# Optimization experiments

Hardware: AMD Instinct MI355X
Metric: run time of the kernel (lower is better)

Reference implementation:

```python
import jax, jax.numpy as jnp
import numpy as np
from jax import lax

BLOCK = 64      # block_size
OVERLAP = 16
NITER = 64      # Niter init kwarg; loop runs min(1000, Niter)
L = 0.24        # diffusion step size
K = 0.03        # exp(logk), logk = log(0.03)
DEPS = 0.1
FFT_STEPS = 10
THRESH = 0.1    # uniform-region variance threshold


def _g(x):
    # g(x) = 1 / (1 + |x^2| / K^2)
    return 1.0 / (1.0 + jnp.abs(x * x) / (K * K))


def _avgpool3(x):
    # F.avg_pool2d(x, 3, stride=1, padding=1) with count_include_pad=True (divide by 9)
    s = lax.reduce_window(x, 0.0, lax.add, (1, 1, 3, 3), (1, 1, 1, 1),
                          [(0, 0), (0, 0), (1, 1), (1, 1)])
    return s / 9.0


def _fft_diffuse_block(block, bcv, bch):
    cv_mean = bcv.mean()
    ch_mean = bch.mean()
    h, w = block.shape[2], block.shape[3]
    ky = jnp.arange(h, dtype=block.dtype)[:, None] * (2.0 * np.pi / h)      # [h,1]
    kx = jnp.arange(w // 2 + 1, dtype=block.dtype)[None, :] * (2.0 * np.pi / w)  # [1,w//2+1]
    op = (1.0 - 2.0 * L * (cv_mean * (1.0 - jnp.cos(ky)) + ch_mean * (1.0 - jnp.cos(kx)))) ** FFT_STEPS
    return jnp.fft.irfft2(jnp.fft.rfft2(block) * op, s=(h, w))


def _forward(guide, initial):
    # depth shift for stability (torch code branches on initial.min() <= deps)
    shift = jnp.where(initial.min() <= DEPS, DEPS, 0.0).astype(initial.dtype)
    depth = initial + shift

    # diffusion coefficients from guide: cv [B,1,H-1,W], ch [B,1,H,W-1]
    cv = _g(jnp.mean(jnp.abs(guide[:, :, 1:, :] - guide[:, :, :-1, :]), axis=1, keepdims=True))
    ch = _g(jnp.mean(jnp.abs(guide[:, :, :, 1:] - guide[:, :, :, :-1]), axis=1, keepdims=True))

    # identify_uniform_regions (local variance via avg pools); original torch code
    # broadcasts shapes (H-1,W) & (H,W-1) which errors -- we crop to common (H-1,W-1)
    cv_var = _avgpool3(cv ** 2) - _avgpool3(cv) ** 2
    ch_var = _avgpool3(ch ** 2) - _avgpool3(ch) ** 2
    uniform = ((cv_var[:, :, :, :-1] < THRESH) & (ch_var[:, :, :-1, :] < THRESH)).astype(depth.dtype)

    B, C, H, W = depth.shape
    step = BLOCK - OVERLAP
    # sequential per-block FFT diffusion with overlap blending (blocks read
    # depth updated by previous blocks, so order matters)
    for b in range(B):
        for y in range(0, H, step):
            for x in range(0, W, step):
                y_end = min(y + BLOCK, H)
                x_end = min(x + BLOCK, W)
                bh, bw = y_end - y, x_end - x
                block = depth[b:b + 1, :, y:y_end, x:x_end]
                bcv = cv[b:b + 1, :, y:y_end - 1, x:x_end]
                bch = ch[b:b + 1, :, y:y_end, x:x_end - 1]
                bun = uniform[b:b + 1, :, y:y_end, x:x_end]  # clips at edges (H-1,W-1)
                cond = bun.mean() > 0.7
                newb = _fft_diffuse_block(block, bcv, bch)
                if y > 0 or x > 0:
                    blend_y = jnp.ones((bh,), depth.dtype)
                    if y > 0:
                        r = jnp.arange(bh)
                        blend_y = jnp.where(r < min(OVERLAP, bh), r.astype(depth.dtype) / OVERLAP, blend_y)
                    blend_x = jnp.ones((bw,), depth.dtype)
                    if x > 0:
                        r = jnp.arange(bw)
                        blend_x = jnp.where(r < min(OVERLAP, bw), r.astype(depth.dtype) / OVERLAP, blend_x)
                    blend = (blend_y[:, None] * blend_x[None, :])[None, None]
                    cand = block * (1.0 - blend) + newb * blend
                else:
                    cand = newb
                region = jnp.where(cond, cand, block)
                depth = depth.at[b:b + 1, :, y:y_end, x:x_end].set(region)

    # explicit anisotropic diffusion stencil, serial data dependence -> lax.scan
    def diffuse_step(I, _):
        dv = I[:, :, 1:, :] - I[:, :, :-1, :]
        dh = I[:, :, :, 1:] - I[:, :, :, :-1]  # computed before vertical update (as in torch)
        tv = L * cv * dv
        I = I.at[:, :, 1:, :].add(-tv).at[:, :, :-1, :].add(tv)
        th = L * ch * dh
        I = I.at[:, :, :, 1:].add(-th).at[:, :, :, :-1].add(th)
        return I, None

    depth, _ = lax.scan(diffuse_step, depth, None, length=min(1000, NITER))
    y_pred = depth - shift
    return y_pred, cv, ch


def setup_inputs() -> dict:
    key = jax.random.key(0)
    k1, k2 = jax.random.split(key)
    guide = jax.random.uniform(k1, (2, 3, 512, 512), dtype=jnp.float32)
    initial = jax.random.uniform(k2, (2, 1, 512, 512), dtype=jnp.float32)
    return {"guide": guide, "initial": initial}


def reference(guide, initial):
    # returns (y_pred, cv, ch) matching {'y_pred':..., 'cv':..., 'ch':...}
    return _forward(guide, initial)
```

## Files before the change

### kernel.cpp

```cpp
#include <hip/hip_runtime.h>
#include <stdint.h>

#define LDIFF 0.24f

constexpr int H = 512, W = 512, NB = 2;
constexpr int HW = H * W;
constexpr int N_D = NB * HW;
constexpr int CVH = 511, CVW = 512;
constexpr int CHH = 512, CHW = 511;
constexpr int N_CV = NB * CVH * CVW;
constexpr int NBLKS = 11;
constexpr int NBT = NB * 121;

__device__ inline float ldc(const float* p) {
    return __hip_atomic_load(p, __ATOMIC_RELAXED, __HIP_MEMORY_SCOPE_AGENT);
}
__device__ inline void stc(float* p, float v) {
    __hip_atomic_store(p, v, __ATOMIC_RELAXED, __HIP_MEMORY_SCOPE_AGENT);
}
__device__ inline void poll_ge(const int* p, int v) {
    while (__hip_atomic_load(p, __ATOMIC_RELAXED, __HIP_MEMORY_SCOPE_AGENT) < v)
        __builtin_amdgcn_s_sleep(2);
}

__device__ inline float rot_a(float x) {
    return __int_as_float(__builtin_amdgcn_update_dpp(0, __float_as_int(x), 0x134, 0xf, 0xf, false));
}
__device__ inline float rot_b(float x) {
    return __int_as_float(__builtin_amdgcn_update_dpp(0, __float_as_int(x), 0x13c, 0xf, 0xf, false));
}
__device__ inline float sh_a(float x) {
    return __int_as_float(__builtin_amdgcn_update_dpp(0, __float_as_int(x), 0x130, 0xf, 0xf, true));
}
__device__ inline float sh_b(float x) {
    return __int_as_float(__builtin_amdgcn_update_dpp(0, __float_as_int(x), 0x138, 0xf, 0xf, true));
}

__global__ __launch_bounds__(256) void kall(
    const float* __restrict__ guide, const float* __restrict__ initial,
    float* __restrict__ cv, float* __restrict__ ch,
    float* __restrict__ D, float* __restrict__ T0, float* __restrict__ T1,
    float* __restrict__ ypred, int* __restrict__ sync_)
{
    __shared__ float pool[8712];
    __shared__ float sm[256];
    __shared__ float prmS[3];
    __shared__ float xT[4][64];
    __shared__ float xB[4][64];
    __shared__ float cvB[4][64];
    float* cvT = pool;
    float* chT = pool + 4356;

    int* wflag = sync_;
    int* dflag = sync_ + 4096;
    int* bar   = sync_ + 8192;

    const int blk = blockIdx.x;
    const int i = blk / NBLKS, j = blk % NBLKS;
    const int b = blockIdx.y;
    const int tid = threadIdx.x;
    const int lane = tid & 63, wv = tid >> 6;
    const int r0 = wv * 16;
    const int me = b * 121 + blk;

    const float kinv = 1.0f / (0.03f * 0.03f);
    for (int idx = me * 256 + tid; idx < N_D; idx += NBT * 256) {
        int bb = idx >> 18;
        int yx = idx & (HW - 1);
        int y = yx >> 9, x = yx & 511;
        const float* g = guide + (size_t)bb * 3 * HW + yx;
        float g0 = g[0], g1 = g[HW], g2 = g[2 * HW];
        stc(&D[idx], initial[idx]);
        if (y < 511) {
            float d = (fabsf(g[512] - g0) + fabsf(g[HW + 512] - g1) + fabsf(g[2 * HW + 512] - g2)) * (1.0f / 3.0f);
            cv[bb * CVH * CVW + y * CVW + x] = 1.0f / (1.0f + d * d * kinv);
        }
        if (x < 511) {
            float d = (fabsf(g[1] - g0) + fabsf(g[HW + 1] - g1) + fabsf(g[2 * HW + 1] - g2)) * (1.0f / 3.0f);
            ch[bb * CHH * CHW + y * CHW + x] = 1.0f / (1.0f + d * d * kinv);
        }
    }

    __syncthreads();
    if (tid == 0) {
        __hip_atomic_fetch_add(bar, 1, __ATOMIC_ACQ_REL, __HIP_MEMORY_SCOPE_AGENT);
        while (__hip_atomic_load(bar, __ATOMIC_RELAXED, __HIP_MEMORY_SCOPE_AGENT) < NBT)
            __builtin_amdgcn_s_sleep(8);
    }
    __syncthreads();
    __builtin_amdgcn_fence(__ATOMIC_ACQUIRE, "agent");

    const int y0 = i * 48, x0 = j * 48;
    const int y1 = min(y0 + 64, 512), x1 = min(x0 + 64, 512);
    const int bh = y1 - y0, bw = x1 - x0;
    const float* cvb = cv + b * CVH * CVW;
    const float* chb = ch + b * CHH * CHW;

    for (int p = tid; p < 66 * 66; p += 256) {
        int rr = p / 66, c2 = p - rr * 66;
        int y = y0 - 1 + rr, x = x0 - 1 + c2;
        cvT[p] = (y >= 0 && y < 511 && x >= 0 && x < 512) ? cvb[y * CVW + x] : 0.0f;
        chT[p] = (y >= 0 && y < 512 && x >= 0 && x < 511) ? chb[y * CHW + x] : 0.0f;
    }
    __syncthreads();

    float scv = 0.f, sch = 0.f, sun = 0.f;
    {
        int n = (bh - 1) * bw;
        for (int p = tid; p < n; p += 256) { int r = p / bw, c = p - r * bw; scv += cvT[(r + 1) * 66 + c + 1]; }
    }
    {
        int cols = bw - 1, n = bh * cols;
        for (int p = tid; p < n; p += 256) { int r = p / cols, c = p - r * cols; sch += chT[(r + 1) * 66 + c + 1]; }
    }
    const int ur = min(y1, 511) - y0, uc = min(x1, 511) - x0;
    {
        int n = ur * uc;
        for (int p = tid; p < n; p += 256) {
            int r = p / uc, c = p - r * uc;
            float s1 = 0.f, s2 = 0.f, t1 = 0.f, t2 = 0.f;
            #pragma unroll
            for (int dy = 0; dy < 3; dy++)
                #pragma unroll
                for (int dx = 0; dx < 3; dx++) {
                    float v = cvT[(r + dy) * 66 + c + dx]; s1 += v; s2 += v * v;
                    float w2 = chT[(r + dy) * 66 + c + dx]; t1 += w2; t2 += w2 * w2;
                }
            float m = s1 * (1.0f / 9.0f);
            float vcv = s2 * (1.0f / 9.0f) - m * m;
            m = t1 * (1.0f / 9.0f);
            float vch = t2 * (1.0f / 9.0f) - m * m;
            if (vcv < 0.1f && vch < 0.1f) sun += 1.f;
        }
    }
    sm[tid] = scv; __syncthreads();
    for (int s = 128; s; s >>= 1) { if (tid < s) sm[tid] += sm[tid + s]; __syncthreads(); }
    if (tid == 0) prmS[0] = sm[0] / (float)((bh - 1) * bw);
    __syncthreads();
    sm[tid] = sch; __syncthreads();
    for (int s = 128; s; s >>= 1) { if (tid < s) sm[tid] += sm[tid + s]; __syncthreads(); }
    if (tid == 0) prmS[1] = sm[0] / (float)(bh * (bw - 1));
    __syncthreads();
    sm[tid] = sun; __syncthreads();
    for (int s = 128; s; s >>= 1) { if (tid < s) sm[tid] += sm[tid + s]; __syncthreads(); }
    if (tid == 0) prmS[2] = (sm[0] / (float)(ur * uc) > 0.7f) ? 1.0f : 0.0f;
    __syncthreads();

    const bool docond = prmS[2] > 0.5f;
    if (tid == 0 && !docond)
        __hip_atomic_store(&wflag[me * 16], 1, __ATOMIC_RELAXED, __HIP_MEMORY_SCOPE_AGENT);

    int pr = __builtin_amdgcn_update_dpp(0, lane, 0x134, 0xf, 0xf, false);
    const bool dirL = (pr == ((lane + 63) & 63));

    float* Db = D + b * HW;
    const float* ini = initial + b * HW;

    if (docond) {
        const float a = LDIFF * prmS[0], bc = LDIFF * prmS[1];
        const int mh = bh - 1, mw = bw - 1;
        const int cc = lane & mw;
        float u[16], orig[16];
        int addr[16]; bool fD[16];
        #pragma unroll
        for (int k = 0; k < 16; k++) {
            int rr = (r0 + k) & mh;
            addr[k] = (y0 + rr) * W + x0 + cc;
            fD[k] = (i > 0 && rr < 16) || (j > 0 && cc < 16);
            if (!fD[k]) orig[k] = ini[addr[k]];
        }
        if (tid < 4) {
            int di = (tid == 0) ? i : i - 1;
            int dj = (tid == 0) ? j - 1 : j - 2 + tid;
            if (di >= 0 && dj >= 0 && dj < NBLKS)
                poll_ge(&wflag[(b * 121 + di * NBLKS + dj) * 16], 1);
        }
        __syncthreads();
        #pragma unroll
        for (int k = 0; k < 16; k++) if (fD[k]) orig[k] = ldc(&Db[addr[k]]);
        #pragma unroll
        for (int k = 0; k < 16; k++) u[k] = orig[k];

        for (int it = 0; it < 10; it++) {
            xT[wv][lane] = u[0];
            xB[wv][lane] = u[15];
            __syncthreads();
            float ub = xB[(wv + 3) & 3][lane];
            float ut = xT[(wv + 1) & 3][lane];
            float nu[16];
            #pragma unroll
            for (int k = 0; k < 16; k++) {
                float up = (k == 0) ? ub : u[k - 1];
                float dn = (k == 15) ? ut : u[k + 1];
                float hsum = rot_a(u[k]) + rot_b(u[k]);
                nu[k] = u[k] + a * (up + dn - 2.0f * u[k]) + bc * (hsum - 2.0f * u[k]);
            }
            #pragma unroll
            for (int k = 0; k < 16; k++) u[k] = nu[k];
            __syncthreads();
        }

        if (lane < bw) {
            float bxw = (x0 > 0 && lane < 16) ? (float)lane * (1.0f / 16.0f) : 1.0f;
            #pragma unroll
            for (int k = 0; k < 16; k++) {
                int r = r0 + k;
                if (r < bh) {
                    float byw = (y0 > 0 && r < 16) ? (float)r * (1.0f / 16.0f) : 1.0f;
                    float wgt = byw * bxw;
                    stc(&Db[(y0 + r) * W + x0 + lane], orig[k] * (1.0f - wgt) + u[k] * wgt);
                }
            }
        }
        asm volatile("s_waitcnt vmcnt(0)" ::: "memory");
        __syncthreads();
        if (tid == 0)
            __hip_atomic_store(&wflag[me * 16], 1, __ATOMIC_RELAXED, __HIP_MEMORY_SCOPE_AGENT);
    }

    const int gy0 = y0 - 8, gx0 = x0 - 8;
    const int cx = gx0 + lane;
    const int gxc = min(max(cx, 0), 511);
    const bool xv = (cx >= 0 && cx < 512);
    float cvr[16], chr[16], chl[16];
    int gyA[16];
    #pragma unroll
    for (int k = 0; k < 16; k++) {
        int cy = gy0 + r0 + k;
        gyA[k] = min(max(cy, 0), 511);
        cvr[k] = (cy >= 0 && cy < 511 && xv) ? cvb[cy * CVW + cx] : 0.0f;
        chr[k] = (cy >= 0 && cy < 512 && xv && cx < 511) ? chb[cy * CHW + cx] : 0.0f;
        chl[k] = dirL ? sh_a(chr[k]) : sh_b(chr[k]);
    }
    cvB[wv][lane] = cvr[15];
    __syncthreads();
    const float cvm1 = (wv == 0) ? 0.0f : cvB[wv - 1][lane];

    float* Tb0 = T0 + b * HW;
    float* Tb1 = T1 + b * HW;
    float* ypb = ypred + b * HW;
    const bool cok = (lane >= 8 && lane < 56 && gx0 + lane < 512);

    for (int t = 1; t <= 8; t++) {
        if (tid < 9) {
            int di = tid / 3 - 1, dj = tid % 3 - 1;
            if (di != 0 || dj != 0) {
                int ni = i + di, nj = j + dj;
                if (ni >= 0 && ni < NBLKS && nj >= 0 && nj < NBLKS) {
                    int nb = (b * 121 + ni * NBLKS + nj) * 16;
                    if (t == 1) poll_ge(&wflag[nb], 1);
                    else        poll_ge(&dflag[nb], t - 1);
                }
            }
        }
        __syncthreads();
        const float* src = (t == 1) ? Db : (((t - 1) & 1) ? Tb1 : Tb0);
        float u[16];
        #pragma unroll
        for (int k = 0; k < 16; k++) u[k] = ldc(&src[gyA[k] * W + gxc]);

        for (int it = 0; it < 8; it++) {
            xT[wv][lane] = u[0];
            xB[wv][lane] = u[15];
            __syncthreads();
            float ub = (wv > 0) ? xB[wv - 1][lane] : u[0];
            float ut = (wv < 3) ? xT[wv + 1][lane] : u[15];
            float V[16];
            #pragma unroll
            for (int k = 0; k < 16; k++) {
                float up = (k == 0) ? ub : u[k - 1];
                float dn = (k == 15) ? ut : u[k + 1];
                float cup = (k == 0) ? cvm1 : cvr[k - 1];
                V[k] = u[k] + LDIFF * cvr[k] * (dn - u[k]) - LDIFF * cup * (u[k] - up);
            }
            #pragma unroll
            for (int k = 0; k < 16; k++) {
                float rA = rot_a(V[k]);
                float rB = rot_b(V[k]);
                float lf = dirL ? rA : rB;
                float rt = dirL ? rB : rA;
                u[k] = V[k] + LDIFF * chr[k] * (rt - V[k]) - LDIFF * chl[k] * (V[k] - lf);
            }
            __syncthreads();
        }

        if (t < 8) {
            float* dst = (t & 1) ? Tb1 : Tb0;
            if (cok) {
                #pragma unroll
                for (int k = 0; k < 16; k++) {
                    int r = r0 + k;
                    if (r >= 8 && r < 56) {
                        int y = gy0 + r;
                        if (y < 512) stc(&dst[y * W + gx0 + lane], u[k]);
                    }
                }
            }
            asm volatile("s_waitcnt vmcnt(0)" ::: "memory");
            __syncthreads();
            if (tid == 0)
                __hip_atomic_store(&dflag[me * 16], t, __ATOMIC_RELAXED, __HIP_MEMORY_SCOPE_AGENT);
        } else {
            if (cok) {
                #pragma unroll
                for (int k = 0; k < 16; k++) {
                    int r = r0 + k;
                    if (r >= 8 && r < 56) {
                        int y = gy0 + r;
                        if (y < 512) ypb[y * W + gx0 + lane] = u[k];
                    }
                }
            }
        }
    }
}

extern "C" void kernel_launch(void* const* d_in, const int* in_sizes, int n_in,
                              void* d_out, int out_size, void* d_ws, size_t ws_size,
                              hipStream_t stream) {
    const float* guide   = (const float*)d_in[0];
    const float* initial = (const float*)d_in[1];
    float* y_pred = (float*)d_out;
    float* cv = y_pred + N_D;
    float* ch = cv + N_CV;

    uint8_t* w = (uint8_t*)d_ws;
    int* sync_ = (int*)w;
    float* D  = (float*)(w + 36864);
    float* T0 = (float*)(w + 36864 + (size_t)N_D * 4);
    float* T1 = (float*)(w + 36864 + (size_t)2 * N_D * 4);

    hipMemsetAsync(sync_, 0, 36864, stream);
    kall<<<dim3(121, NB), 256, 0, stream>>>(guide, initial, cv, ch, D, T0, T1, y_pred, sync_);
}
```

Measured before the change: 351.3 us.

## Serialize block-row FFT phase in one workgroup per row with LDS strip handoff

The sequential per-block smoothing phase is reassigned so that the first workgroup of each block row processes all 11 blocks of that row in order. Other workgroups publish their block statistics through a global parameter queue, and the row worker passes the 16-column overlap strip to the next block through shared memory. Per-block flags are replaced by per-row progress counters, which removes cross-workgroup flag round trips and repeated global reloads of the overlap region. In exchange, most workgroups sit idle while the row workers run serially, and the stencil phase now waits on row progress instead of neighbouring block flags.

Result: slower. 449.1 us (+27.8%).

```diff
diff --git a/kernel.cpp b/kernel.cpp
--- a/kernel.cpp
+++ b/kernel.cpp
@@ -18,9 +18,15 @@
 __device__ inline void stc(float* p, float v) {
     __hip_atomic_store(p, v, __ATOMIC_RELAXED, __HIP_MEMORY_SCOPE_AGENT);
 }
+__device__ inline int ldci(const int* p) {
+    return __hip_atomic_load(p, __ATOMIC_RELAXED, __HIP_MEMORY_SCOPE_AGENT);
+}
+__device__ inline void stci(int* p, int v) {
+    __hip_atomic_store(p, v, __ATOMIC_RELAXED, __HIP_MEMORY_SCOPE_AGENT);
+}
+template <int SLP>
 __device__ inline void poll_ge(const int* p, int v) {
-    while (__hip_atomic_load(p, __ATOMIC_RELAXED, __HIP_MEMORY_SCOPE_AGENT) < v)
-        __builtin_amdgcn_s_sleep(2);
+    while (ldci(p) < v) __builtin_amdgcn_s_sleep(SLP);
 }
 
 __device__ inline float rot_a(float x) {
@@ -44,16 +50,18 @@
 {
     __shared__ float pool[8712];
     __shared__ float sm[256];
-    __shared__ float prmS[3];
+    __shared__ float prmS[4];
     __shared__ float xT[4][64];
     __shared__ float xB[4][64];
     __shared__ float cvB[4][64];
+    __shared__ float stripS[64][16];
     float* cvT = pool;
     float* chT = pool + 4356;
 
-    int* wflag = sync_;
-    int* dflag = sync_ + 4096;
-    int* bar   = sync_ + 8192;
+    int* bar     = sync_;
+    int* rowflag = sync_ + 16;
+    int* dflag   = sync_ + 512;
+    int* prmq    = sync_ + 4608;
 
     const int blk = blockIdx.x;
     const int i = blk / NBLKS, j = blk % NBLKS;
@@ -84,8 +92,7 @@
     __syncthreads();
     if (tid == 0) {
         __hip_atomic_fetch_add(bar, 1, __ATOMIC_ACQ_REL, __HIP_MEMORY_SCOPE_AGENT);
-        while (__hip_atomic_load(bar, __ATOMIC_RELAXED, __HIP_MEMORY_SCOPE_AGENT) < NBT)
-            __builtin_amdgcn_s_sleep(8);
+        while (ldci(bar) < NBT) __builtin_amdgcn_s_sleep(8);
     }
     __syncthreads();
     __builtin_amdgcn_fence(__ATOMIC_ACQUIRE, "agent");
@@ -146,76 +153,95 @@
     if (tid == 0) prmS[2] = (sm[0] / (float)(ur * uc) > 0.7f) ? 1.0f : 0.0f;
     __syncthreads();
 
-    const bool docond = prmS[2] > 0.5f;
-    if (tid == 0 && !docond)
-        __hip_atomic_store(&wflag[me * 16], 1, __ATOMIC_RELAXED, __HIP_MEMORY_SCOPE_AGENT);
-
     int pr = __builtin_amdgcn_update_dpp(0, lane, 0x134, 0xf, 0xf, false);
     const bool dirL = (pr == ((lane + 63) & 63));
 
     float* Db = D + b * HW;
-    const float* ini = initial + b * HW;
-
-    if (docond) {
-        const float a = LDIFF * prmS[0], bc = LDIFF * prmS[1];
-        const int mh = bh - 1, mw = bw - 1;
-        const int cc = lane & mw;
-        float u[16], orig[16];
-        int addr[16]; bool fD[16];
-        #pragma unroll
-        for (int k = 0; k < 16; k++) {
-            int rr = (r0 + k) & mh;
-            addr[k] = (y0 + rr) * W + x0 + cc;
-            fD[k] = (i > 0 && rr < 16) || (j > 0 && cc < 16);
-            if (!fD[k]) orig[k] = ini[addr[k]];
-        }
-        if (tid < 4) {
-            int di = (tid == 0) ? i : i - 1;
-            int dj = (tid == 0) ? j - 1 : j - 2 + tid;
-            if (di >= 0 && dj >= 0 && dj < NBLKS)
-                poll_ge(&wflag[(b * 121 + di * NBLKS + dj) * 16], 1);
-        }
-        __syncthreads();
-        #pragma unroll
-        for (int k = 0; k < 16; k++) if (fD[k]) orig[k] = ldc(&Db[addr[k]]);
-        #pragma unroll
-        for (int k = 0; k < 16; k++) u[k] = orig[k];
-
-        for (int it = 0; it < 10; it++) {
-            xT[wv][lane] = u[0];
-            xB[wv][lane] = u[15];
-            __syncthreads();
-            float ub = xB[(wv + 3) & 3][lane];
-            float ut = xT[(wv + 1) & 3][lane];
-            float nu[16];
-            #pragma unroll
-            for (int k = 0; k < 16; k++) {
-                float up = (k == 0) ? ub : u[k - 1];
-                float dn = (k == 15) ? ut : u[k + 1];
-                float hsum = rot_a(u[k]) + rot_b(u[k]);
-                nu[k] = u[k] + a * (up + dn - 2.0f * u[k]) + bc * (hsum - 2.0f * u[k]);
-            }
-            #pragma unroll
-            for (int k = 0; k < 16; k++) u[k] = nu[k];
-            __syncthreads();
-        }
-
-        if (lane < bw) {
-            float bxw = (x0 > 0 && lane < 16) ? (float)lane * (1.0f / 16.0f) : 1.0f;
-            #pragma unroll
-            for (int k = 0; k < 16; k++) {
-                int r = r0 + k;
-                if (r < bh) {
-                    float byw = (y0 > 0 && r < 16) ? (float)r * (1.0f / 16.0f) : 1.0f;
+
+    if (j == 0) {
+        const int bhR = bh;
+        const int mh = bhR - 1;
+        const int rfme = (b * 11 + i) * 16;
+        for (int jj = 0; jj <= 10; jj++) {
+            const int x0j = jj * 48;
+            const int bwj = (jj == 10) ? 32 : 64;
+            const int mw = bwj - 1;
+            const int cc = lane & mw;
+            if (jj > 0) {
+                if (tid == 0) {
+                    int* q = prmq + (b * 121 + i * NBLKS + jj) * 8;
+                    while (ldci(&q[3]) == 0) __builtin_amdgcn_s_sleep(2);
+                    prmS[0] = __int_as_float(ldci(&q[0]));
+                    prmS[1] = __int_as_float(ldci(&q[1]));
+                    prmS[2] = __int_as_float(ldci(&q[2]));
+                }
+            }
+            if (i > 0 && tid == 1)
+                poll_ge<2>(&rowflag[(b * 11 + i - 1) * 16], min(jj + 2, 11));
+            __syncthreads();
+            const bool cond = prmS[2] > 0.5f;
+            const float a = LDIFF * prmS[0], bc = LDIFF * prmS[1];
+
+            if (cond) {
+                float u[16], orig[16];
+                #pragma unroll
+                for (int k = 0; k < 16; k++) {
+                    int rr = (r0 + k) & mh;
+                    orig[k] = (jj > 0 && cc < 16) ? stripS[r0 + k][cc]
+                                                  : ldc(&Db[(y0 + rr) * W + x0j + cc]);
+                    u[k] = orig[k];
+                }
+                for (int it = 0; it < 10; it++) {
+                    xT[wv][lane] = u[0];
+                    xB[wv][lane] = u[15];
+                    __syncthreads();
+                    float ub = xB[(wv + 3) & 3][lane];
+                    float ut = xT[(wv + 1) & 3][lane];
+                    float nu[16];
+                    #pragma unroll
+                    for (int k = 0; k < 16; k++) {
+                        float up = (k == 0) ? ub : u[k - 1];
+                        float dn = (k == 15) ? ut : u[k + 1];
+                        float hsum = rot_a(u[k]) + rot_b(u[k]);
+                        nu[k] = u[k] + a * (up + dn - 2.0f * u[k]) + bc * (hsum - 2.0f * u[k]);
+                    }
+                    #pragma unroll
+                    for (int k = 0; k < 16; k++) u[k] = nu[k];
+                    __syncthreads();
+                }
+                #pragma unroll
+                for (int k = 0; k < 16; k++) {
+                    int rr = (r0 + k) & mh;
+                    float byw = (y0 > 0 && rr < 16) ? (float)rr * (1.0f / 16.0f) : 1.0f;
+                    float bxw = (x0j > 0 && cc < 16) ? (float)cc * (1.0f / 16.0f) : 1.0f;
                     float wgt = byw * bxw;
-                    stc(&Db[(y0 + r) * W + x0 + lane], orig[k] * (1.0f - wgt) + u[k] * wgt);
-                }
-            }
-        }
-        asm volatile("s_waitcnt vmcnt(0)" ::: "memory");
-        __syncthreads();
-        if (tid == 0)
-            __hip_atomic_store(&wflag[me * 16], 1, __ATOMIC_RELAXED, __HIP_MEMORY_SCOPE_AGENT);
+                    float val = orig[k] * (1.0f - wgt) + u[k] * wgt;
+                    if ((r0 + k) < bhR && lane < bwj)
+                        stc(&Db[(y0 + r0 + k) * W + x0j + lane], val);
+                    if (jj < 10 && lane >= 48) stripS[r0 + k][lane - 48] = val;
+                }
+            } else {
+                if (jj < 10 && lane >= 48) {
+                    #pragma unroll
+                    for (int k = 0; k < 16; k++) {
+                        int rr = (r0 + k) & mh;
+                        stripS[r0 + k][lane - 48] = ldc(&Db[(y0 + rr) * W + x0j + lane]);
+                    }
+                }
+            }
+            asm volatile("s_waitcnt vmcnt(0)" ::: "memory");
+            __syncthreads();
+            if (tid == 0) stci(&rowflag[rfme], jj + 1);
+        }
+    } else {
+        if (tid == 0) {
+            int* q = prmq + me * 8;
+            stci(&q[0], __float_as_int(prmS[0]));
+            stci(&q[1], __float_as_int(prmS[1]));
+            stci(&q[2], __float_as_int(prmS[2]));
+            asm volatile("s_waitcnt vmcnt(0)" ::: "memory");
+            stci(&q[3], 1);
+        }
     }
 
     const int gy0 = y0 - 8, gx0 = x0 - 8;
@@ -242,14 +268,16 @@
     const bool cok = (lane >= 8 && lane < 56 && gx0 + lane < 512);
 
     for (int t = 1; t <= 8; t++) {
-        if (tid < 9) {
-            int di = tid / 3 - 1, dj = tid % 3 - 1;
-            if (di != 0 || dj != 0) {
-                int ni = i + di, nj = j + dj;
-                if (ni >= 0 && ni < NBLKS && nj >= 0 && nj < NBLKS) {
-                    int nb = (b * 121 + ni * NBLKS + nj) * 16;
-                    if (t == 1) poll_ge(&wflag[nb], 1);
-                    else        poll_ge(&dflag[nb], t - 1);
+        if (t == 1) {
+            if (tid == 0)
+                poll_ge<8>(&rowflag[(b * 11 + min(i + 1, 10)) * 16], min(j + 2, 11));
+        } else {
+            if (tid < 9) {
+                int di = tid / 3 - 1, dj = tid % 3 - 1;
+                if (di != 0 || dj != 0) {
+                    int ni = i + di, nj = j + dj;
+                    if (ni >= 0 && ni < NBLKS && nj >= 0 && nj < NBLKS)
+                        poll_ge<2>(&dflag[(b * 121 + ni * NBLKS + nj) * 16], t - 1);
                 }
             }
         }
@@ -298,8 +326,7 @@
             }
             asm volatile("s_waitcnt vmcnt(0)" ::: "memory");
             __syncthreads();
-            if (tid == 0)
-                __hip_atomic_store(&dflag[me * 16], t, __ATOMIC_RELAXED, __HIP_MEMORY_SCOPE_AGENT);
+            if (tid == 0) stci(&dflag[me * 16], t);
         } else {
             if (cok) {
                 #pragma unroll
@@ -326,10 +353,10 @@
 
     uint8_t* w = (uint8_t*)d_ws;
     int* sync_ = (int*)w;
-    float* D  = (float*)(w + 36864);
-    float* T0 = (float*)(w + 36864 + (size_t)N_D * 4);
-    float* T1 = (float*)(w + 36864 + (size_t)2 * N_D * 4);
-
-    hipMemsetAsync(sync_, 0, 36864, stream);
+    float* D  = (float*)(w + 32768);
+    float* T0 = (float*)(w + 32768 + (size_t)N_D * 4);
+    float* T1 = (float*)(w + 32768 + (size_t)2 * N_D * 4);
+
+    (void)hipMemsetAsync(sync_, 0, 28672, stream);
     kall<<<dim3(121, NB), 256, 0, stream>>>(guide, initial, cv, ch, D, T0, T1, y_pred, sync_);
 }
```

## Compute coefficients per tile with halo to drop the global grid barrier

Applied to the files above, without the earlier changes.

Each workgroup now computes cv/ch for its own 73x73 haloed tile straight from the guide into shared memory, writes its owned part of cv/ch, and initializes its own region of D. This removes the global atomic barrier and the full-image pre-pass. The diffusion loops use double-buffered shared halo exchange to drop one __syncthreads per iteration, and the block reductions use wave shuffles. In exchange, guide reads and coefficient math are duplicated in overlapping halos, and correctness now depends on neighbour-flag polling to order the writes to D.

After: 322.1 us. 1.09x faster.

```diff
diff --git a/kernel.cpp b/kernel.cpp
--- a/kernel.cpp
+++ b/kernel.cpp
@@ -18,9 +18,15 @@
 __device__ inline void stc(float* p, float v) {
     __hip_atomic_store(p, v, __ATOMIC_RELAXED, __HIP_MEMORY_SCOPE_AGENT);
 }
+__device__ inline int ldci(const int* p) {
+    return __hip_atomic_load(p, __ATOMIC_RELAXED, __HIP_MEMORY_SCOPE_AGENT);
+}
+__device__ inline void stci(int* p, int v) {
+    __hip_atomic_store(p, v, __ATOMIC_RELAXED, __HIP_MEMORY_SCOPE_AGENT);
+}
+template <int SLP>
 __device__ inline void poll_ge(const int* p, int v) {
-    while (__hip_atomic_load(p, __ATOMIC_RELAXED, __HIP_MEMORY_SCOPE_AGENT) < v)
-        __builtin_amdgcn_s_sleep(2);
+    while (ldci(p) < v) __builtin_amdgcn_s_sleep(SLP);
 }
 
 __device__ inline float rot_a(float x) {
@@ -42,18 +48,15 @@
     float* __restrict__ D, float* __restrict__ T0, float* __restrict__ T1,
     float* __restrict__ ypred, int* __restrict__ sync_)
 {
-    __shared__ float pool[8712];
-    __shared__ float sm[256];
+    __shared__ float cvT[73 * 74];
+    __shared__ float chT[73 * 74];
+    __shared__ float xT[2][4][64];
+    __shared__ float xB[2][4][64];
+    __shared__ float red[12];
     __shared__ float prmS[3];
-    __shared__ float xT[4][64];
-    __shared__ float xB[4][64];
-    __shared__ float cvB[4][64];
-    float* cvT = pool;
-    float* chT = pool + 4356;
 
     int* wflag = sync_;
     int* dflag = sync_ + 4096;
-    int* bar   = sync_ + 8192;
 
     const int blk = blockIdx.x;
     const int i = blk / NBLKS, j = blk % NBLKS;
@@ -63,55 +66,57 @@
     const int r0 = wv * 16;
     const int me = b * 121 + blk;
 
-    const float kinv = 1.0f / (0.03f * 0.03f);
-    for (int idx = me * 256 + tid; idx < N_D; idx += NBT * 256) {
-        int bb = idx >> 18;
-        int yx = idx & (HW - 1);
-        int y = yx >> 9, x = yx & 511;
-        const float* g = guide + (size_t)bb * 3 * HW + yx;
-        float g0 = g[0], g1 = g[HW], g2 = g[2 * HW];
-        stc(&D[idx], initial[idx]);
-        if (y < 511) {
-            float d = (fabsf(g[512] - g0) + fabsf(g[HW + 512] - g1) + fabsf(g[2 * HW + 512] - g2)) * (1.0f / 3.0f);
-            cv[bb * CVH * CVW + y * CVW + x] = 1.0f / (1.0f + d * d * kinv);
-        }
-        if (x < 511) {
-            float d = (fabsf(g[1] - g0) + fabsf(g[HW + 1] - g1) + fabsf(g[2 * HW + 1] - g2)) * (1.0f / 3.0f);
-            ch[bb * CHH * CHW + y * CHW + x] = 1.0f / (1.0f + d * d * kinv);
-        }
-    }
-
-    __syncthreads();
-    if (tid == 0) {
-        __hip_atomic_fetch_add(bar, 1, __ATOMIC_ACQ_REL, __HIP_MEMORY_SCOPE_AGENT);
-        while (__hip_atomic_load(bar, __ATOMIC_RELAXED, __HIP_MEMORY_SCOPE_AGENT) < NBT)
-            __builtin_amdgcn_s_sleep(8);
-    }
-    __syncthreads();
-    __builtin_amdgcn_fence(__ATOMIC_ACQUIRE, "agent");
-
     const int y0 = i * 48, x0 = j * 48;
     const int y1 = min(y0 + 64, 512), x1 = min(x0 + 64, 512);
     const int bh = y1 - y0, bw = x1 - x0;
-    const float* cvb = cv + b * CVH * CVW;
-    const float* chb = ch + b * CHH * CHW;
-
-    for (int p = tid; p < 66 * 66; p += 256) {
-        int rr = p / 66, c2 = p - rr * 66;
-        int y = y0 - 1 + rr, x = x0 - 1 + c2;
-        cvT[p] = (y >= 0 && y < 511 && x >= 0 && x < 512) ? cvb[y * CVW + x] : 0.0f;
-        chT[p] = (y >= 0 && y < 512 && x >= 0 && x < 511) ? chb[y * CHW + x] : 0.0f;
+    const int yb = y0 - 8, xb = x0 - 8;
+    const float kinv = 1.0f / (0.03f * 0.03f);
+
+    const float* gb = guide + (size_t)b * 3 * HW;
+    for (int p = tid; p < 73 * 73; p += 256) {
+        int rr = p / 73, cc2 = p - rr * 73;
+        int y = yb + rr, x = xb + cc2;
+        float cvv = 0.0f, chv = 0.0f;
+        if (y >= 0 && y < 512 && x >= 0 && x < 512) {
+            const float* g = gb + y * W + x;
+            float g0 = g[0], g1 = g[HW], g2 = g[2 * HW];
+            if (y < 511) {
+                float d = (fabsf(g[W] - g0) + fabsf(g[HW + W] - g1) + fabsf(g[2 * HW + W] - g2)) * (1.0f / 3.0f);
+                cvv = 1.0f / (1.0f + d * d * kinv);
+            }
+            if (x < 511) {
+                float d = (fabsf(g[1] - g0) + fabsf(g[HW + 1] - g1) + fabsf(g[2 * HW + 1] - g2)) * (1.0f / 3.0f);
+                chv = 1.0f / (1.0f + d * d * kinv);
+            }
+        }
+        cvT[rr * 74 + cc2] = cvv;
+        chT[rr * 74 + cc2] = chv;
     }
     __syncthreads();
+
+    {
+        int rcv = min(y0 + 48, CVH) - y0, ccv = min(x0 + 48, CVW) - x0;
+        float* cvo = cv + b * CVH * CVW;
+        for (int p = tid; p < rcv * ccv; p += 256) {
+            int r = p / ccv, c = p - r * ccv;
+            cvo[(y0 + r) * CVW + x0 + c] = cvT[(r + 8) * 74 + c + 8];
+        }
+        int rch = min(y0 + 48, CHH) - y0, cch = min(x0 + 48, CHW) - x0;
+        float* cho = ch + b * CHH * CHW;
+        for (int p = tid; p < rch * cch; p += 256) {
+            int r = p / cch, c = p - r * cch;
+            cho[(y0 + r) * CHW + x0 + c] = chT[(r + 8) * 74 + c + 8];
+        }
+    }
 
     float scv = 0.f, sch = 0.f, sun = 0.f;
     {
         int n = (bh - 1) * bw;
-        for (int p = tid; p < n; p += 256) { int r = p / bw, c = p - r * bw; scv += cvT[(r + 1) * 66 + c + 1]; }
+        for (int p = tid; p < n; p += 256) { int r = p / bw, c = p - r * bw; scv += cvT[(r + 8) * 74 + c + 8]; }
     }
     {
         int cols = bw - 1, n = bh * cols;
-        for (int p = tid; p < n; p += 256) { int r = p / cols, c = p - r * cols; sch += chT[(r + 1) * 66 + c + 1]; }
+        for (int p = tid; p < n; p += 256) { int r = p / cols, c = p - r * cols; sch += chT[(r + 8) * 74 + c + 8]; }
     }
     const int ur = min(y1, 511) - y0, uc = min(x1, 511) - x0;
     {
@@ -123,8 +128,8 @@
             for (int dy = 0; dy < 3; dy++)
                 #pragma unroll
                 for (int dx = 0; dx < 3; dx++) {
-                    float v = cvT[(r + dy) * 66 + c + dx]; s1 += v; s2 += v * v;
-                    float w2 = chT[(r + dy) * 66 + c + dx]; t1 += w2; t2 += w2 * w2;
+                    float v = cvT[(r + 7 + dy) * 74 + c + 7 + dx]; s1 += v; s2 += v * v;
+                    float w2 = chT[(r + 7 + dy) * 74 + c + 7 + dx]; t1 += w2; t2 += w2 * w2;
                 }
             float m = s1 * (1.0f / 9.0f);
             float vcv = s2 * (1.0f / 9.0f) - m * m;
@@ -133,47 +138,62 @@
             if (vcv < 0.1f && vch < 0.1f) sun += 1.f;
         }
     }
-    sm[tid] = scv; __syncthreads();
-    for (int s = 128; s; s >>= 1) { if (tid < s) sm[tid] += sm[tid + s]; __syncthreads(); }
-    if (tid == 0) prmS[0] = sm[0] / (float)((bh - 1) * bw);
+    #pragma unroll
+    for (int m = 1; m < 64; m <<= 1) {
+        scv += __shfl_xor(scv, m);
+        sch += __shfl_xor(sch, m);
+        sun += __shfl_xor(sun, m);
+    }
+    if (lane == 0) { red[wv * 3] = scv; red[wv * 3 + 1] = sch; red[wv * 3 + 2] = sun; }
     __syncthreads();
-    sm[tid] = sch; __syncthreads();
-    for (int s = 128; s; s >>= 1) { if (tid < s) sm[tid] += sm[tid + s]; __syncthreads(); }
-    if (tid == 0) prmS[1] = sm[0] / (float)(bh * (bw - 1));
+    if (tid == 0) {
+        float a0 = red[0] + red[3] + red[6] + red[9];
+        float a1 = red[1] + red[4] + red[7] + red[10];
+        float a2 = red[2] + red[5] + red[8] + red[11];
+        prmS[0] = a0 / (float)((bh - 1) * bw);
+        prmS[1] = a1 / (float)(bh * (bw - 1));
+        prmS[2] = (a2 / (float)(ur * uc) > 0.7f) ? 1.0f : 0.0f;
+    }
     __syncthreads();
-    sm[tid] = sun; __syncthreads();
-    for (int s = 128; s; s >>= 1) { if (tid < s) sm[tid] += sm[tid + s]; __syncthreads(); }
-    if (tid == 0) prmS[2] = (sm[0] / (float)(ur * uc) > 0.7f) ? 1.0f : 0.0f;
-    __syncthreads();
-
-    const bool docond = prmS[2] > 0.5f;
-    if (tid == 0 && !docond)
-        __hip_atomic_store(&wflag[me * 16], 1, __ATOMIC_RELAXED, __HIP_MEMORY_SCOPE_AGENT);
-
-    int pr = __builtin_amdgcn_update_dpp(0, lane, 0x134, 0xf, 0xf, false);
-    const bool dirL = (pr == ((lane + 63) & 63));
-
+
+    int prb = __builtin_amdgcn_update_dpp(0, lane, 0x134, 0xf, 0xf, false);
+    const bool dirL = (prb == ((lane + 63) & 63));
+
+    const bool cond = prmS[2] > 0.5f;
+    const float a = LDIFF * prmS[0], bc = LDIFF * prmS[1];
     float* Db = D + b * HW;
     const float* ini = initial + b * HW;
 
-    if (docond) {
-        const float a = LDIFF * prmS[0], bc = LDIFF * prmS[1];
-        const int mh = bh - 1, mw = bw - 1;
-        const int cc = lane & mw;
+    const int mh = bh - 1, mw = bw - 1;
+    const int ccw = lane & mw;
+
+    if (!cond) {
+        #pragma unroll
+        for (int k = 0; k < 16; k++) {
+            int r = r0 + k;
+            if (r < bh && (i == 0 || r >= 16) && lane < bw && (j == 0 || lane >= 16)) {
+                int ad = (y0 + r) * W + x0 + lane;
+                stc(&Db[ad], ini[ad]);
+            }
+        }
+        asm volatile("s_waitcnt vmcnt(0)" ::: "memory");
+        __syncthreads();
+        if (tid == 0) stci(&wflag[me * 16], 1);
+    } else {
         float u[16], orig[16];
         int addr[16]; bool fD[16];
         #pragma unroll
         for (int k = 0; k < 16; k++) {
             int rr = (r0 + k) & mh;
-            addr[k] = (y0 + rr) * W + x0 + cc;
-            fD[k] = (i > 0 && rr < 16) || (j > 0 && cc < 16);
+            addr[k] = (y0 + rr) * W + x0 + ccw;
+            fD[k] = (i > 0 && rr < 16) || (j > 0 && ccw < 16);
             if (!fD[k]) orig[k] = ini[addr[k]];
         }
-        if (tid < 4) {
+        if (tid < 3) {
             int di = (tid == 0) ? i : i - 1;
-            int dj = (tid == 0) ? j - 1 : j - 2 + tid;
+            int dj = (tid == 0) ? j - 1 : ((tid == 1) ? j : j + 1);
             if (di >= 0 && dj >= 0 && dj < NBLKS)
-                poll_ge(&wflag[(b * 121 + di * NBLKS + dj) * 16], 1);
+                poll_ge<1>(&wflag[(b * 121 + di * NBLKS + dj) * 16], 1);
         }
         __syncthreads();
         #pragma unroll
@@ -181,12 +201,13 @@
         #pragma unroll
         for (int k = 0; k < 16; k++) u[k] = orig[k];
 
+        int bs = 0;
         for (int it = 0; it < 10; it++) {
-            xT[wv][lane] = u[0];
-            xB[wv][lane] = u[15];
+            xT[bs][wv][lane] = u[0];
+            xB[bs][wv][lane] = u[15];
             __syncthreads();
-            float ub = xB[(wv + 3) & 3][lane];
-            float ut = xT[(wv + 1) & 3][lane];
+            float ub = xB[bs][(wv + 3) & 3][lane];
+            float ut = xT[bs][(wv + 1) & 3][lane];
             float nu[16];
             #pragma unroll
             for (int k = 0; k < 16; k++) {
@@ -197,74 +218,68 @@
             }
             #pragma unroll
             for (int k = 0; k < 16; k++) u[k] = nu[k];
-            __syncthreads();
-        }
-
-        if (lane < bw) {
-            float bxw = (x0 > 0 && lane < 16) ? (float)lane * (1.0f / 16.0f) : 1.0f;
-            #pragma unroll
-            for (int k = 0; k < 16; k++) {
-                int r = r0 + k;
-                if (r < bh) {
-                    float byw = (y0 > 0 && r < 16) ? (float)r * (1.0f / 16.0f) : 1.0f;
-                    float wgt = byw * bxw;
-                    stc(&Db[(y0 + r) * W + x0 + lane], orig[k] * (1.0f - wgt) + u[k] * wgt);
-                }
+            bs ^= 1;
+        }
+
+        #pragma unroll
+        for (int k = 0; k < 16; k++) {
+            int r = r0 + k;
+            if (r < bh && lane < bw) {
+                int rr = r;
+                float byw = (y0 > 0 && rr < 16) ? (float)rr * (1.0f / 16.0f) : 1.0f;
+                float bxw = (x0 > 0 && lane < 16) ? (float)lane * (1.0f / 16.0f) : 1.0f;
+                float wgt = byw * bxw;
+                stc(&Db[(y0 + r) * W + x0 + lane], orig[k] * (1.0f - wgt) + u[k] * wgt);
             }
         }
         asm volatile("s_waitcnt vmcnt(0)" ::: "memory");
         __syncthreads();
-        if (tid == 0)
-            __hip_atomic_store(&wflag[me * 16], 1, __ATOMIC_RELAXED, __HIP_MEMORY_SCOPE_AGENT);
-    }
-
-    const int gy0 = y0 - 8, gx0 = x0 - 8;
-    const int cx = gx0 + lane;
+        if (tid == 0) stci(&wflag[me * 16], 1);
+    }
+
+    const int cx = xb + lane;
     const int gxc = min(max(cx, 0), 511);
-    const bool xv = (cx >= 0 && cx < 512);
     float cvr[16], chr[16], chl[16];
     int gyA[16];
     #pragma unroll
     for (int k = 0; k < 16; k++) {
-        int cy = gy0 + r0 + k;
+        int cy = yb + r0 + k;
         gyA[k] = min(max(cy, 0), 511);
-        cvr[k] = (cy >= 0 && cy < 511 && xv) ? cvb[cy * CVW + cx] : 0.0f;
-        chr[k] = (cy >= 0 && cy < 512 && xv && cx < 511) ? chb[cy * CHW + cx] : 0.0f;
+        cvr[k] = cvT[(r0 + k) * 74 + lane];
+        chr[k] = chT[(r0 + k) * 74 + lane];
         chl[k] = dirL ? sh_a(chr[k]) : sh_b(chr[k]);
     }
-    cvB[wv][lane] = cvr[15];
-    __syncthreads();
-    const float cvm1 = (wv == 0) ? 0.0f : cvB[wv - 1][lane];
+    const float cvm1 = (wv == 0) ? 0.0f : cvT[(r0 - 1) * 74 + lane];
 
     float* Tb0 = T0 + b * HW;
     float* Tb1 = T1 + b * HW;
     float* ypb = ypred + b * HW;
-    const bool cok = (lane >= 8 && lane < 56 && gx0 + lane < 512);
+    const bool cok = (lane >= 8 && lane < 56 && xb + lane < 512);
 
     for (int t = 1; t <= 8; t++) {
         if (tid < 9) {
             int di = tid / 3 - 1, dj = tid % 3 - 1;
-            if (di != 0 || dj != 0) {
-                int ni = i + di, nj = j + dj;
-                if (ni >= 0 && ni < NBLKS && nj >= 0 && nj < NBLKS) {
-                    int nb = (b * 121 + ni * NBLKS + nj) * 16;
-                    if (t == 1) poll_ge(&wflag[nb], 1);
-                    else        poll_ge(&dflag[nb], t - 1);
-                }
-            }
-        }
+            int ni = i + di, nj = j + dj;
+            if (ni >= 0 && ni < NBLKS && nj >= 0 && nj < NBLKS && (di | dj) != 0) {
+                int nb = (b * 121 + ni * NBLKS + nj) * 16;
+                if (t == 1) poll_ge<2>(&wflag[nb], 1);
+                else        poll_ge<2>(&dflag[nb], t - 1);
+            }
+        }
+        if (t == 1 && tid == 9) poll_ge<2>(&wflag[me * 16], 1);
         __syncthreads();
         const float* src = (t == 1) ? Db : (((t - 1) & 1) ? Tb1 : Tb0);
         float u[16];
         #pragma unroll
         for (int k = 0; k < 16; k++) u[k] = ldc(&src[gyA[k] * W + gxc]);
 
+        int bs = 0;
         for (int it = 0; it < 8; it++) {
-            xT[wv][lane] = u[0];
-            xB[wv][lane] = u[15];
+            xT[bs][wv][lane] = u[0];
+            xB[bs][wv][lane] = u[15];
             __syncthreads();
-            float ub = (wv > 0) ? xB[wv - 1][lane] : u[0];
-            float ut = (wv < 3) ? xT[wv + 1][lane] : u[15];
+            float ub = (wv > 0) ? xB[bs][wv - 1][lane] : u[0];
+            float ut = (wv < 3) ? xT[bs][wv + 1][lane] : u[15];
             float V[16];
             #pragma unroll
             for (int k = 0; k < 16; k++) {
@@ -281,7 +296,7 @@
                 float rt = dirL ? rB : rA;
                 u[k] = V[k] + LDIFF * chr[k] * (rt - V[k]) - LDIFF * chl[k] * (V[k] - lf);
             }
-            __syncthreads();
+            bs ^= 1;
         }
 
         if (t < 8) {
@@ -291,23 +306,22 @@
                 for (int k = 0; k < 16; k++) {
                     int r = r0 + k;
                     if (r >= 8 && r < 56) {
-                        int y = gy0 + r;
-                        if (y < 512) stc(&dst[y * W + gx0 + lane], u[k]);
+                        int y = yb + r;
+                        if (y < 512) stc(&dst[y * W + xb + lane], u[k]);
                     }
                 }
             }
             asm volatile("s_waitcnt vmcnt(0)" ::: "memory");
             __syncthreads();
-            if (tid == 0)
-                __hip_atomic_store(&dflag[me * 16], t, __ATOMIC_RELAXED, __HIP_MEMORY_SCOPE_AGENT);
+            if (tid == 0) stci(&dflag[me * 16], t);
         } else {
             if (cok) {
                 #pragma unroll
                 for (int k = 0; k < 16; k++) {
                     int r = r0 + k;
                     if (r >= 8 && r < 56) {
-                        int y = gy0 + r;
-                        if (y < 512) ypb[y * W + gx0 + lane] = u[k];
+                        int y = yb + r;
+                        if (y < 512) ypb[y * W + xb + lane] = u[k];
                     }
                 }
             }
@@ -326,10 +340,10 @@
 
     uint8_t* w = (uint8_t*)d_ws;
     int* sync_ = (int*)w;
-    float* D  = (float*)(w + 36864);
-    float* T0 = (float*)(w + 36864 + (size_t)N_D * 4);
-    float* T1 = (float*)(w + 36864 + (size_t)2 * N_D * 4);
-
-    hipMemsetAsync(sync_, 0, 36864, stream);
+    float* D  = (float*)(w + 32768);
+    float* T0 = (float*)(w + 32768 + (size_t)N_D * 4);
+    float* T1 = (float*)(w + 32768 + (size_t)2 * N_D * 4);
+
+    (void)hipMemsetAsync(sync_, 0, 32768, stream);
     kall<<<dim3(121, NB), 256, 0, stream>>>(guide, initial, cv, ch, D, T0, T1, y_pred, sync_);
 }
```
